# Kernel tuning notes

Measured on AMD Instinct MI355X. Metric: run time of the kernel, lower is better.

Reference implementation:

```python
import jax, jax.numpy as jnp
import numpy as np

N_NODES = 50000
N_EDGES = 800000
IN_FEATS, HIDDEN, OUT = 256, 64, 32


def graph_conv(x, W, b, src, dst, n_nodes):
    # DGL GraphConv with norm='both': h = D_in^{-1/2} A D_out^{-1/2} (x W) + b
    ones = jnp.ones((src.shape[0],), dtype=x.dtype)
    deg_out = jax.ops.segment_sum(ones, src, num_segments=n_nodes)
    deg_in = jax.ops.segment_sum(ones, dst, num_segments=n_nodes)
    norm_out = jax.lax.rsqrt(jnp.maximum(deg_out, 1.0))  # [N]
    norm_in = jax.lax.rsqrt(jnp.maximum(deg_in, 1.0))    # [N]
    xw = x @ W                                # [N, out] dense transform first
    msg = (xw * norm_out[:, None])[src]       # [E, out] gather
    agg = jax.ops.segment_sum(msg, dst, num_segments=n_nodes)  # [N, out]
    return agg * norm_in[:, None] + b


def setup_inputs() -> dict:
    key = jax.random.key(0)
    ks = jax.random.split(key, 9)
    inputs = jax.random.normal(ks[0], (N_NODES, IN_FEATS), dtype=jnp.float32)
    src = jax.random.randint(ks[1], (N_EDGES,), 0, N_NODES)
    dst = jax.random.randint(ks[2], (N_EDGES,), 0, N_NODES)
    W1 = jax.random.normal(ks[3], (IN_FEATS, HIDDEN), dtype=jnp.float32) / np.sqrt(IN_FEATS)
    b1 = jnp.zeros((HIDDEN,), dtype=jnp.float32)
    W2 = jax.random.normal(ks[4], (HIDDEN, OUT), dtype=jnp.float32) / np.sqrt(HIDDEN)
    b2 = jnp.zeros((OUT,), dtype=jnp.float32)
    fc_w = jax.random.normal(ks[5], (N_NODES,), dtype=jnp.float32) / np.sqrt(N_NODES)
    fc_b = jnp.zeros((1,), dtype=jnp.float32)
    return {"inputs": inputs, "src": src, "dst": dst,
            "W1": W1, "b1": b1, "W2": W2, "b2": b2,
            "fc_w": fc_w, "fc_b": fc_b}


def reference(inputs, src, dst, W1, b1, W2, b2, fc_w, fc_b):
    g1 = jax.nn.relu(graph_conv(inputs, W1, b1, src, dst, N_NODES))  # [N, H]
    g2 = jax.nn.relu(graph_conv(g1, W2, b2, src, dst, N_NODES))      # [N, O]
    # fc(g2.t()): Linear(nodes, 1) on [O, N] -> [O, 1]
    out = jnp.einsum('no,n->o', g2, fc_w)[:, None] + fc_b
    return out
```

## Files before the change

kernel.cpp:

```cpp
#include <hip/hip_runtime.h>

#define N_NODES 50000
#define N_EDGES 800000
#define IN_FEATS 256
#define HIDDEN 64
#define OUTF 32
#define SCAN_BLOCKS 196

#define NSLICE 64
#define SLICE_E 12500
#define NRANGE 4
#define RANGE_N 12800
#define PSTRIDE 51200

#define HRANGE 2
#define HRANGE_N 25600

typedef __attribute__((ext_vector_type(8))) short bf16x8;
typedef __attribute__((ext_vector_type(4))) float f32x4;
typedef unsigned short u16;

__device__ __forceinline__ unsigned f2bf_pk(float a, float b) {
    union { float f; unsigned u; } x, y;
    x.f = a; y.f = b;
    unsigned lo = x.u + 0x7FFFu + ((x.u >> 16) & 1u);
    unsigned hi = y.u + 0x7FFFu + ((y.u >> 16) & 1u);
    return (lo >> 16) | (hi & 0xFFFF0000u);
}
__device__ __forceinline__ u16 f2bf(float a) {
    union { float f; unsigned u; } x;
    x.f = a;
    return (u16)((x.u + 0x7FFFu + ((x.u >> 16) & 1u)) >> 16);
}
__device__ __forceinline__ float bf2f(u16 h) {
    union { unsigned u; float f; } x;
    x.u = ((unsigned)h) << 16;
    return x.f;
}

__global__ __launch_bounds__(512) void hist_kernel(const int* __restrict__ src,
                                                   const int* __restrict__ dst,
                                                   unsigned char* __restrict__ partial) {
    __shared__ int h[HRANGE_N / 2];
    const int bid = blockIdx.x;
    const int which = bid & 1;
    const int r = (bid >> 1) & 1;
    const int s = bid >> 2;
    const int tid = threadIdx.x;
    const int lo = r * HRANGE_N;

    for (int i = tid; i < HRANGE_N / 2; i += 512) h[i] = 0;
    __syncthreads();

    const int* arr = which ? dst : src;
    const int e0 = s * SLICE_E;
    for (int j = tid; j < SLICE_E; j += 512) {
        int v = arr[e0 + j] - lo;
        if ((unsigned)v < HRANGE_N) atomicAdd(&h[v >> 1], 1 << ((v & 1) << 4));
    }
    __syncthreads();

    unsigned char* p = partial + (size_t)which * NSLICE * PSTRIDE + (size_t)s * PSTRIDE + lo;
    for (int i = tid; i < HRANGE_N / 2; i += 512) {
        int c = h[i];
        p[i * 2 + 0] = (unsigned char)(c & 0xFFFF);
        p[i * 2 + 1] = (unsigned char)((unsigned)c >> 16);
    }
}

__global__ __launch_bounds__(256) void reduce_scan_kernel(unsigned char* __restrict__ partial,
                                                          int* __restrict__ row_start,
                                                          int* __restrict__ block_sums,
                                                          float* __restrict__ norm_out,
                                                          float* __restrict__ norm_in) {
    __shared__ int sh[256];
    int i = blockIdx.x * 256 + threadIdx.x;
    int run = 0;
    if (i < N_NODES) {
        const unsigned char* ps = partial + i;
        unsigned char* pd = partial + (size_t)NSLICE * PSTRIDE + i;
        int so = 0;
#pragma unroll 8
        for (int s = 0; s < NSLICE; ++s) so += ps[(size_t)s * PSTRIDE];
        norm_out[i] = rsqrtf(fmaxf((float)so, 1.0f));
#pragma unroll 8
        for (int s = 0; s < NSLICE; ++s) {
            int c = pd[(size_t)s * PSTRIDE];
            pd[(size_t)s * PSTRIDE] = (unsigned char)run;
            run += c;
        }
        norm_in[i] = rsqrtf(fmaxf((float)run, 1.0f));
    }
    sh[threadIdx.x] = run;
    __syncthreads();
#pragma unroll
    for (int off = 1; off < 256; off <<= 1) {
        int t = (threadIdx.x >= off) ? sh[threadIdx.x - off] : 0;
        __syncthreads();
        sh[threadIdx.x] += t;
        __syncthreads();
    }
    if (i < N_NODES) row_start[i] = sh[threadIdx.x] - run;
    if (threadIdx.x == 255) block_sums[blockIdx.x] = sh[255];
}

__global__ __launch_bounds__(256) void scan3_kernel(int* __restrict__ row_start,
                                                    const int* __restrict__ block_sums) {
    __shared__ int s[256];
    int v = (threadIdx.x < SCAN_BLOCKS) ? block_sums[threadIdx.x] : 0;
    s[threadIdx.x] = v;
    __syncthreads();
#pragma unroll
    for (int off = 1; off < 256; off <<= 1) {
        int t = (threadIdx.x >= off) ? s[threadIdx.x - off] : 0;
        __syncthreads();
        s[threadIdx.x] += t;
        __syncthreads();
    }
    int base = (blockIdx.x == 0) ? 0 : s[blockIdx.x - 1];
    int i = blockIdx.x * 256 + threadIdx.x;
    if (i < N_NODES) row_start[i] += base;
    if (i == 0) row_start[N_NODES] = N_EDGES;
}

__global__ __launch_bounds__(512) void fill_csr_kernel(const int* __restrict__ src,
                                                       const int* __restrict__ dst,
                                                       const int* __restrict__ row_start,
                                                       const unsigned char* __restrict__ rel,
                                                       int* __restrict__ csr_src) {
    __shared__ int cur[RANGE_N];
    const int bid = blockIdx.x;
    const int r = bid & 3;
    const int s = bid >> 2;
    const int tid = threadIdx.x;
    const int lo = r * RANGE_N;

    const unsigned char* relp = rel + (size_t)s * PSTRIDE;
    for (int i = tid; i < RANGE_N; i += 512) {
        int node = lo + i;
        cur[i] = (node < N_NODES) ? row_start[node] + (int)relp[node] : 0;
    }
    __syncthreads();

    const int e0 = s * SLICE_E;
    for (int j = tid; j < SLICE_E; j += 512) {
        int d = dst[e0 + j] - lo;
        if ((unsigned)d < RANGE_N) {
            int pos = atomicAdd(&cur[d], 1);
            csr_src[pos] = src[e0 + j];
        }
    }
}

#define AST 136
__global__ __launch_bounds__(256) void gemm1_kernel(const float* __restrict__ x,
                                                    const float* __restrict__ W1,
                                                    const float* __restrict__ norm_out,
                                                    u16* __restrict__ xw1) {
    __shared__ short As[64 * AST];
    __shared__ short Bt[64 * AST];
    const int tid = threadIdx.x;
    const int n0 = blockIdx.x * 64;

    const f32x4 zero4 = {0.f, 0.f, 0.f, 0.f};
    f32x4 acc[4] = {zero4, zero4, zero4, zero4};

    const int srow = tid >> 2;
    const int sseg = tid & 3;
    const int grow = n0 + srow;
    const bool grow_ok = grow < N_NODES;

    const int w = tid >> 6;
    const int l = tid & 63;

    for (int c = 0; c < 2; ++c) {
        if (c) __syncthreads();
        {
            const float* xp = x + (size_t)grow * IN_FEATS + c * 128 + sseg * 32;
            short* ap = As + srow * AST + sseg * 32;
#pragma unroll
            for (int j = 0; j < 8; ++j) {
                float4 v = make_float4(0.f, 0.f, 0.f, 0.f);
                if (grow_ok) v = *(const float4*)(xp + j * 4);
                unsigned p0 = f2bf_pk(v.x, v.y);
                unsigned p1 = f2bf_pk(v.z, v.w);
                *(uint2*)(ap + j * 4) = make_uint2(p0, p1);
            }
        }
        {
#pragma unroll
            for (int it = 0; it < 16; ++it) {
                int flat = tid + it * 256;
                int kp = flat >> 6;
                int col = flat & 63;
                int k = c * 128 + kp * 2;
                float w0 = W1[(size_t)k * HIDDEN + col];
                float w1 = W1[(size_t)(k + 1) * HIDDEN + col];
                *(unsigned*)(Bt + col * AST + kp * 2) = f2bf_pk(w0, w1);
            }
        }
        __syncthreads();

        const short* ap = As + (w * 16 + (l & 15)) * AST + (l >> 4) * 8;
        const short* bp = Bt + (l & 15) * AST + (l >> 4) * 8;
#pragma unroll
        for (int ks = 0; ks < 4; ++ks) {
            bf16x8 af = *(const bf16x8*)(ap + ks * 32);
#pragma unroll
            for (int ct = 0; ct < 4; ++ct) {
                bf16x8 bfv = *(const bf16x8*)(bp + ct * 16 * AST + ks * 32);
                acc[ct] = __builtin_amdgcn_mfma_f32_16x16x32_bf16(af, bfv, acc[ct], 0, 0, 0);
            }
        }
    }

    const int rbase = n0 + w * 16 + (l >> 4) * 4;
    const int cbase = l & 15;
#pragma unroll
    for (int j = 0; j < 4; ++j) {
        int row = rbase + j;
        if (row < N_NODES) {
            float nrm = norm_out[row];
            u16* orow = xw1 + (size_t)row * HIDDEN + cbase;
#pragma unroll
            for (int ct = 0; ct < 4; ++ct)
                orow[ct * 16] = f2bf(acc[ct][j] * nrm);
        }
    }
}

__global__ __launch_bounds__(256) void gemm2_kernel(const float* __restrict__ g1,
                                                    const float* __restrict__ W2,
                                                    const float* __restrict__ norm_out,
                                                    u16* __restrict__ xw2) {
    __shared__ float gs[8][HIDDEN];
    __shared__ float ws[HIDDEN * OUTF];
    const int tid = threadIdx.x;
    const int n0 = blockIdx.x * 8;

#pragma unroll
    for (int i = 0; i < 8; ++i) ws[tid + i * 256] = W2[tid + i * 256];
    const float4* gv = (const float4*)(g1 + (size_t)n0 * HIDDEN);
    if (tid < 128) ((float4*)&gs[0][0])[tid] = gv[tid];
    __syncthreads();

    const int o = tid & 31;
    const int r = tid >> 5;
    float acc = 0.f;
#pragma unroll
    for (int k = 0; k < HIDDEN; ++k) acc += gs[r][k] * ws[k * OUTF + o];
    xw2[(size_t)(n0 + r) * OUTF + o] = f2bf(acc * norm_out[n0 + r]);
}

__global__ __launch_bounds__(256) void gather64_kernel(const int* __restrict__ row_start,
                                                       const int* __restrict__ csr_src,
                                                       const u16* __restrict__ xw,
                                                       const float* __restrict__ norm_in,
                                                       const float* __restrict__ b,
                                                       float* __restrict__ g) {
    int n = blockIdx.x * 4 + (threadIdx.x >> 6);
    if (n >= N_NODES) return;
    int lane = threadIdx.x & 63;
    int beg = row_start[n], end = row_start[n + 1];
    float acc = 0.f;
    int i = beg;
    for (; i + 8 <= end; i += 8) {
        int s0 = csr_src[i + 0], s1 = csr_src[i + 1];
        int s2 = csr_src[i + 2], s3 = csr_src[i + 3];
        int s4 = csr_src[i + 4], s5 = csr_src[i + 5];
        int s6 = csr_src[i + 6], s7 = csr_src[i + 7];
        float v0 = bf2f(xw[(size_t)s0 * 64 + lane]);
        float v1 = bf2f(xw[(size_t)s1 * 64 + lane]);
        float v2 = bf2f(xw[(size_t)s2 * 64 + lane]);
        float v3 = bf2f(xw[(size_t)s3 * 64 + lane]);
        float v4 = bf2f(xw[(size_t)s4 * 64 + lane]);
        float v5 = bf2f(xw[(size_t)s5 * 64 + lane]);
        float v6 = bf2f(xw[(size_t)s6 * 64 + lane]);
        float v7 = bf2f(xw[(size_t)s7 * 64 + lane]);
        acc += ((v0 + v1) + (v2 + v3)) + ((v4 + v5) + (v6 + v7));
    }
    for (; i < end; ++i) acc += bf2f(xw[(size_t)csr_src[i] * 64 + lane]);
    g[(size_t)n * 64 + lane] = fmaxf(acc * norm_in[n] + b[lane], 0.f);
}

__global__ __launch_bounds__(256) void gather32_kernel(const int* __restrict__ row_start,
                                                       const int* __restrict__ csr_src,
                                                       const u16* __restrict__ xw,
                                                       const float* __restrict__ norm_in,
                                                       const float* __restrict__ b,
                                                       float* __restrict__ g) {
    int n = blockIdx.x * 8 + (threadIdx.x >> 5);
    if (n >= N_NODES) return;
    int lane = threadIdx.x & 31;
    int beg = row_start[n], end = row_start[n + 1];
    float acc = 0.f;
    int i = beg;
    for (; i + 8 <= end; i += 8) {
        int s0 = csr_src[i + 0], s1 = csr_src[i + 1];
        int s2 = csr_src[i + 2], s3 = csr_src[i + 3];
        int s4 = csr_src[i + 4], s5 = csr_src[i + 5];
        int s6 = csr_src[i + 6], s7 = csr_src[i + 7];
        float v0 = bf2f(xw[(size_t)s0 * 32 + lane]);
        float v1 = bf2f(xw[(size_t)s1 * 32 + lane]);
        float v2 = bf2f(xw[(size_t)s2 * 32 + lane]);
        float v3 = bf2f(xw[(size_t)s3 * 32 + lane]);
        float v4 = bf2f(xw[(size_t)s4 * 32 + lane]);
        float v5 = bf2f(xw[(size_t)s5 * 32 + lane]);
        float v6 = bf2f(xw[(size_t)s6 * 32 + lane]);
        float v7 = bf2f(xw[(size_t)s7 * 32 + lane]);
        acc += ((v0 + v1) + (v2 + v3)) + ((v4 + v5) + (v6 + v7));
    }
    for (; i < end; ++i) acc += bf2f(xw[(size_t)csr_src[i] * 32 + lane]);
    g[(size_t)n * 32 + lane] = fmaxf(acc * norm_in[n] + b[lane], 0.f);
}

__global__ __launch_bounds__(32) void init_out_kernel(float* __restrict__ out,
                                                      const float* __restrict__ fc_b) {
    out[threadIdx.x] = fc_b[0];
}

__global__ __launch_bounds__(256) void reduce_kernel(const float* __restrict__ g2,
                                                     const float* __restrict__ fc_w,
                                                     float* __restrict__ out) {
    __shared__ float s[OUTF];
    const int tid = threadIdx.x;
    if (tid < OUTF) s[tid] = 0.f;
    __syncthreads();

    const int f4 = tid & 7;
    int n = blockIdx.x * 32 + (tid >> 3);
    const int stride = gridDim.x * 32;
    float ax = 0.f, ay = 0.f, az = 0.f, aw = 0.f;
    for (; n < N_NODES; n += stride) {
        float w = fc_w[n];
        float4 g = ((const float4*)(g2 + (size_t)n * OUTF))[f4];
        ax += g.x * w; ay += g.y * w; az += g.z * w; aw += g.w * w;
    }
    atomicAdd(&s[f4 * 4 + 0], ax);
    atomicAdd(&s[f4 * 4 + 1], ay);
    atomicAdd(&s[f4 * 4 + 2], az);
    atomicAdd(&s[f4 * 4 + 3], aw);
    __syncthreads();
    if (tid < OUTF) atomicAdd(&out[tid], s[tid]);
}

extern "C" void kernel_launch(void* const* d_in, const int* in_sizes, int n_in,
                              void* d_out, int out_size, void* d_ws, size_t ws_size,
                              hipStream_t stream) {
    const float* x    = (const float*)d_in[0];
    const int*   src  = (const int*)d_in[1];
    const int*   dst  = (const int*)d_in[2];
    const float* W1   = (const float*)d_in[3];
    const float* b1   = (const float*)d_in[4];
    const float* W2   = (const float*)d_in[5];
    const float* b2   = (const float*)d_in[6];
    const float* fc_w = (const float*)d_in[7];
    const float* fc_b = (const float*)d_in[8];
    float* out = (float*)d_out;

    int* ip = (int*)d_ws;
    int* csr_src      = ip;
    int* row_start    = ip + 800000;
    int* block_sums   = ip + 850001;
    float* fp = (float*)(ip + 850260);
    u16* xw_buf     = (u16*)fp;
    float* g_buf    = fp + 3200000;
    float* norm_out = fp + 6400000;
    float* norm_in  = fp + 6450000;
    unsigned char* partial = (unsigned char*)(fp + 6500000);
    unsigned char* rel = partial + (size_t)NSLICE * PSTRIDE;

    hist_kernel<<<NSLICE * HRANGE * 2, 512, 0, stream>>>(src, dst, partial);
    reduce_scan_kernel<<<SCAN_BLOCKS, 256, 0, stream>>>(partial, row_start, block_sums,
                                                        norm_out, norm_in);
    scan3_kernel<<<SCAN_BLOCKS, 256, 0, stream>>>(row_start, block_sums);
    fill_csr_kernel<<<NSLICE * NRANGE, 512, 0, stream>>>(src, dst, row_start, rel, csr_src);

    gemm1_kernel<<<(N_NODES + 63) / 64, 256, 0, stream>>>(x, W1, norm_out, xw_buf);
    gather64_kernel<<<(N_NODES + 3) / 4, 256, 0, stream>>>(row_start, csr_src, xw_buf,
                                                           norm_in, b1, g_buf);

    gemm2_kernel<<<N_NODES / 8, 256, 0, stream>>>(g_buf, W2, norm_out, xw_buf);
    gather32_kernel<<<(N_NODES + 7) / 8, 256, 0, stream>>>(row_start, csr_src, xw_buf,
                                                           norm_in, b2, g_buf);

    init_out_kernel<<<1, 32, 0, stream>>>(out, fc_b);
    reduce_kernel<<<512, 256, 0, stream>>>(g_buf, fc_w, out);
}
```

Measured before the change: 160.8 us.

## Fuse gathers with gemm2 and final reduction, use 16-bit CSR indices

The layer-1 gather is fused with the layer-2 dense transform, so the hidden features stay in shared memory instead of passing through a global fp32 buffer. The layer-2 gather is fused with the fc reduction, so g2 is never written to global memory. CSR source indices are stored as u16, which is valid only because the node count is below 65536. Gathers now load two bf16 values per lane and split edges across half-waves, with shuffle reductions to combine them. Together these remove two kernel launches and several global round trips, at the cost of more complex indexing and extra shuffles.

```diff
diff --git a/kernel.cpp b/kernel.cpp
--- a/kernel.cpp
+++ b/kernel.cpp
@@ -32,10 +32,11 @@
     x.f = a;
     return (u16)((x.u + 0x7FFFu + ((x.u >> 16) & 1u)) >> 16);
 }
-__device__ __forceinline__ float bf2f(u16 h) {
-    union { unsigned u; float f; } x;
-    x.u = ((unsigned)h) << 16;
-    return x.f;
+__device__ __forceinline__ float bflo(unsigned v) {
+    union { unsigned u; float f; } x; x.u = v << 16; return x.f;
+}
+__device__ __forceinline__ float bfhi(unsigned v) {
+    union { unsigned u; float f; } x; x.u = v & 0xFFFF0000u; return x.f;
 }
 
 __global__ __launch_bounds__(512) void hist_kernel(const int* __restrict__ src,
@@ -127,7 +128,7 @@
                                                        const int* __restrict__ dst,
                                                        const int* __restrict__ row_start,
                                                        const unsigned char* __restrict__ rel,
-                                                       int* __restrict__ csr_src) {
+                                                       u16* __restrict__ csr16) {
     __shared__ int cur[RANGE_N];
     const int bid = blockIdx.x;
     const int r = bid & 3;
@@ -147,7 +148,7 @@
         int d = dst[e0 + j] - lo;
         if ((unsigned)d < RANGE_N) {
             int pos = atomicAdd(&cur[d], 1);
-            csr_src[pos] = src[e0 + j];
+            csr16[pos] = (u16)src[e0 + j];
         }
     }
 }
@@ -229,119 +230,143 @@
     }
 }
 
-__global__ __launch_bounds__(256) void gemm2_kernel(const float* __restrict__ g1,
-                                                    const float* __restrict__ W2,
-                                                    const float* __restrict__ norm_out,
-                                                    u16* __restrict__ xw2) {
-    __shared__ float gs[8][HIDDEN];
+__global__ __launch_bounds__(256) void gather64_gemm2_kernel(const int* __restrict__ row_start,
+                                                             const u16* __restrict__ csr16,
+                                                             const u16* __restrict__ xw1,
+                                                             const float* __restrict__ norm_in,
+                                                             const float* __restrict__ b1,
+                                                             const float* __restrict__ W2,
+                                                             const float* __restrict__ norm_out,
+                                                             u16* __restrict__ xw2) {
+    __shared__ float gs[16][68];
     __shared__ float ws[HIDDEN * OUTF];
     const int tid = threadIdx.x;
-    const int n0 = blockIdx.x * 8;
-
 #pragma unroll
     for (int i = 0; i < 8; ++i) ws[tid + i * 256] = W2[tid + i * 256];
-    const float4* gv = (const float4*)(g1 + (size_t)n0 * HIDDEN);
-    if (tid < 128) ((float4*)&gs[0][0])[tid] = gv[tid];
+
+    const int w = tid >> 6;
+    const int l = tid & 63;
+    const int p = l & 31;
+    const int gsl = l >> 5;
+    const int n0 = blockIdx.x * 16;
+
+#pragma unroll
+    for (int i4 = 0; i4 < 4; ++i4) {
+        int nl = w * 4 + i4;
+        int n = n0 + nl;
+        int beg = row_start[n], end = row_start[n + 1];
+        float ax = 0.f, ay = 0.f;
+        int i = beg;
+        for (; i + 8 <= end; i += 8) {
+            int s0 = csr16[i + gsl];
+            int s1 = csr16[i + 2 + gsl];
+            int s2 = csr16[i + 4 + gsl];
+            int s3 = csr16[i + 6 + gsl];
+            unsigned v0 = *(const unsigned*)(xw1 + (size_t)s0 * 64 + 2 * p);
+            unsigned v1 = *(const unsigned*)(xw1 + (size_t)s1 * 64 + 2 * p);
+            unsigned v2 = *(const unsigned*)(xw1 + (size_t)s2 * 64 + 2 * p);
+            unsigned v3 = *(const unsigned*)(xw1 + (size_t)s3 * 64 + 2 * p);
+            ax += (bflo(v0) + bflo(v1)) + (bflo(v2) + bflo(v3));
+            ay += (bfhi(v0) + bfhi(v1)) + (bfhi(v2) + bfhi(v3));
+        }
+        for (; i + 2 <= end; i += 2) {
+            int s0 = csr16[i + gsl];
+            unsigned v0 = *(const unsigned*)(xw1 + (size_t)s0 * 64 + 2 * p);
+            ax += bflo(v0);
+            ay += bfhi(v0);
+        }
+        if (i < end && gsl == 0) {
+            int s0 = csr16[i];
+            unsigned v0 = *(const unsigned*)(xw1 + (size_t)s0 * 64 + 2 * p);
+            ax += bflo(v0);
+            ay += bfhi(v0);
+        }
+        ax += __shfl_xor(ax, 32);
+        ay += __shfl_xor(ay, 32);
+        if (gsl == 0) {
+            float nin = norm_in[n];
+            gs[nl][2 * p]     = fmaxf(ax * nin + b1[2 * p], 0.f);
+            gs[nl][2 * p + 1] = fmaxf(ay * nin + b1[2 * p + 1], 0.f);
+        }
+    }
     __syncthreads();
 
     const int o = tid & 31;
     const int r = tid >> 5;
-    float acc = 0.f;
-#pragma unroll
-    for (int k = 0; k < HIDDEN; ++k) acc += gs[r][k] * ws[k * OUTF + o];
-    xw2[(size_t)(n0 + r) * OUTF + o] = f2bf(acc * norm_out[n0 + r]);
-}
-
-__global__ __launch_bounds__(256) void gather64_kernel(const int* __restrict__ row_start,
-                                                       const int* __restrict__ csr_src,
-                                                       const u16* __restrict__ xw,
-                                                       const float* __restrict__ norm_in,
-                                                       const float* __restrict__ b,
-                                                       float* __restrict__ g) {
-    int n = blockIdx.x * 4 + (threadIdx.x >> 6);
-    if (n >= N_NODES) return;
-    int lane = threadIdx.x & 63;
-    int beg = row_start[n], end = row_start[n + 1];
-    float acc = 0.f;
-    int i = beg;
-    for (; i + 8 <= end; i += 8) {
-        int s0 = csr_src[i + 0], s1 = csr_src[i + 1];
-        int s2 = csr_src[i + 2], s3 = csr_src[i + 3];
-        int s4 = csr_src[i + 4], s5 = csr_src[i + 5];
-        int s6 = csr_src[i + 6], s7 = csr_src[i + 7];
-        float v0 = bf2f(xw[(size_t)s0 * 64 + lane]);
-        float v1 = bf2f(xw[(size_t)s1 * 64 + lane]);
-        float v2 = bf2f(xw[(size_t)s2 * 64 + lane]);
-        float v3 = bf2f(xw[(size_t)s3 * 64 + lane]);
-        float v4 = bf2f(xw[(size_t)s4 * 64 + lane]);
-        float v5 = bf2f(xw[(size_t)s5 * 64 + lane]);
-        float v6 = bf2f(xw[(size_t)s6 * 64 + lane]);
-        float v7 = bf2f(xw[(size_t)s7 * 64 + lane]);
-        acc += ((v0 + v1) + (v2 + v3)) + ((v4 + v5) + (v6 + v7));
-    }
-    for (; i < end; ++i) acc += bf2f(xw[(size_t)csr_src[i] * 64 + lane]);
-    g[(size_t)n * 64 + lane] = fmaxf(acc * norm_in[n] + b[lane], 0.f);
-}
-
-__global__ __launch_bounds__(256) void gather32_kernel(const int* __restrict__ row_start,
-                                                       const int* __restrict__ csr_src,
-                                                       const u16* __restrict__ xw,
-                                                       const float* __restrict__ norm_in,
-                                                       const float* __restrict__ b,
-                                                       float* __restrict__ g) {
-    int n = blockIdx.x * 8 + (threadIdx.x >> 5);
-    if (n >= N_NODES) return;
-    int lane = threadIdx.x & 31;
-    int beg = row_start[n], end = row_start[n + 1];
-    float acc = 0.f;
-    int i = beg;
-    for (; i + 8 <= end; i += 8) {
-        int s0 = csr_src[i + 0], s1 = csr_src[i + 1];
-        int s2 = csr_src[i + 2], s3 = csr_src[i + 3];
-        int s4 = csr_src[i + 4], s5 = csr_src[i + 5];
-        int s6 = csr_src[i + 6], s7 = csr_src[i + 7];
-        float v0 = bf2f(xw[(size_t)s0 * 32 + lane]);
-        float v1 = bf2f(xw[(size_t)s1 * 32 + lane]);
-        float v2 = bf2f(xw[(size_t)s2 * 32 + lane]);
-        float v3 = bf2f(xw[(size_t)s3 * 32 + lane]);
-        float v4 = bf2f(xw[(size_t)s4 * 32 + lane]);
-        float v5 = bf2f(xw[(size_t)s5 * 32 + lane]);
-        float v6 = bf2f(xw[(size_t)s6 * 32 + lane]);
-        float v7 = bf2f(xw[(size_t)s7 * 32 + lane]);
-        acc += ((v0 + v1) + (v2 + v3)) + ((v4 + v5) + (v6 + v7));
-    }
-    for (; i < end; ++i) acc += bf2f(xw[(size_t)csr_src[i] * 32 + lane]);
-    g[(size_t)n * 32 + lane] = fmaxf(acc * norm_in[n] + b[lane], 0.f);
+    float a0 = 0.f, a1 = 0.f;
+#pragma unroll 8
+    for (int k = 0; k < 64; ++k) {
+        float wv = ws[k * 32 + o];
+        a0 += gs[r][k] * wv;
+        a1 += gs[r + 8][k] * wv;
+    }
+    int row0 = n0 + r, row1 = n0 + r + 8;
+    xw2[(size_t)row0 * 32 + o] = f2bf(a0 * norm_out[row0]);
+    xw2[(size_t)row1 * 32 + o] = f2bf(a1 * norm_out[row1]);
+}
+
+__global__ __launch_bounds__(256) void gather32_reduce_kernel(const int* __restrict__ row_start,
+                                                              const u16* __restrict__ csr16,
+                                                              const u16* __restrict__ xw2,
+                                                              const float* __restrict__ norm_in,
+                                                              const float* __restrict__ b2,
+                                                              const float* __restrict__ fc_w,
+                                                              float* __restrict__ out) {
+    __shared__ float sout[OUTF];
+    const int tid = threadIdx.x;
+    if (tid < OUTF) sout[tid] = 0.f;
+    __syncthreads();
+
+    const int w = tid >> 6;
+    const int l = tid & 63;
+    const int p = l & 15;
+    const int gsl = l >> 4;
+    float tx = 0.f, ty = 0.f;
+
+    for (int n = blockIdx.x * 4 + w; n < N_NODES; n += gridDim.x * 4) {
+        int beg = row_start[n], end = row_start[n + 1];
+        float ax = 0.f, ay = 0.f;
+        int i = beg;
+        for (; i + 8 <= end; i += 8) {
+            int s0 = csr16[i + gsl];
+            int s1 = csr16[i + 4 + gsl];
+            unsigned v0 = *(const unsigned*)(xw2 + (size_t)s0 * 32 + 2 * p);
+            unsigned v1 = *(const unsigned*)(xw2 + (size_t)s1 * 32 + 2 * p);
+            ax += bflo(v0) + bflo(v1);
+            ay += bfhi(v0) + bfhi(v1);
+        }
+        for (; i + 4 <= end; i += 4) {
+            int s0 = csr16[i + gsl];
+            unsigned v0 = *(const unsigned*)(xw2 + (size_t)s0 * 32 + 2 * p);
+            ax += bflo(v0);
+            ay += bfhi(v0);
+        }
+        int t = end - i;
+        if (gsl < t) {
+            int s0 = csr16[i + gsl];
+            unsigned v0 = *(const unsigned*)(xw2 + (size_t)s0 * 32 + 2 * p);
+            ax += bflo(v0);
+            ay += bfhi(v0);
+        }
+        ax += __shfl_xor(ax, 16); ax += __shfl_xor(ax, 32);
+        ay += __shfl_xor(ay, 16); ay += __shfl_xor(ay, 32);
+        if (gsl == 0) {
+            float nin = norm_in[n], fw = fc_w[n];
+            tx += fmaxf(ax * nin + b2[2 * p], 0.f) * fw;
+            ty += fmaxf(ay * nin + b2[2 * p + 1], 0.f) * fw;
+        }
+    }
+    if (gsl == 0) {
+        atomicAdd(&sout[2 * p], tx);
+        atomicAdd(&sout[2 * p + 1], ty);
+    }
+    __syncthreads();
+    if (tid < OUTF) atomicAdd(&out[tid], sout[tid]);
 }
 
 __global__ __launch_bounds__(32) void init_out_kernel(float* __restrict__ out,
                                                       const float* __restrict__ fc_b) {
     out[threadIdx.x] = fc_b[0];
-}
-
-__global__ __launch_bounds__(256) void reduce_kernel(const float* __restrict__ g2,
-                                                     const float* __restrict__ fc_w,
-                                                     float* __restrict__ out) {
-    __shared__ float s[OUTF];
-    const int tid = threadIdx.x;
-    if (tid < OUTF) s[tid] = 0.f;
-    __syncthreads();
-
-    const int f4 = tid & 7;
-    int n = blockIdx.x * 32 + (tid >> 3);
-    const int stride = gridDim.x * 32;
-    float ax = 0.f, ay = 0.f, az = 0.f, aw = 0.f;
-    for (; n < N_NODES; n += stride) {
-        float w = fc_w[n];
-        float4 g = ((const float4*)(g2 + (size_t)n * OUTF))[f4];
-        ax += g.x * w; ay += g.y * w; az += g.z * w; aw += g.w * w;
-    }
-    atomicAdd(&s[f4 * 4 + 0], ax);
-    atomicAdd(&s[f4 * 4 + 1], ay);
-    atomicAdd(&s[f4 * 4 + 2], az);
-    atomicAdd(&s[f4 * 4 + 3], aw);
-    __syncthreads();
-    if (tid < OUTF) atomicAdd(&out[tid], s[tid]);
 }
 
 extern "C" void kernel_launch(void* const* d_in, const int* in_sizes, int n_in,
@@ -358,32 +383,29 @@
     const float* fc_b = (const float*)d_in[8];
     float* out = (float*)d_out;
 
-    int* ip = (int*)d_ws;
-    int* csr_src      = ip;
-    int* row_start    = ip + 800000;
-    int* block_sums   = ip + 850001;
-    float* fp = (float*)(ip + 850260);
-    u16* xw_buf     = (u16*)fp;
-    float* g_buf    = fp + 3200000;
-    float* norm_out = fp + 6400000;
-    float* norm_in  = fp + 6450000;
-    unsigned char* partial = (unsigned char*)(fp + 6500000);
+    u16* csr16      = (u16*)d_ws;
+    int* row_start  = (int*)(csr16 + 800000);
+    int* block_sums = row_start + 50004;
+    u16* xw1_buf    = (u16*)(block_sums + 260);
+    u16* xw2_buf    = xw1_buf + 3200000;
+    float* norm_out = (float*)(xw2_buf + 1600000);
+    float* norm_in  = norm_out + 50000;
+    unsigned char* partial = (unsigned char*)(norm_in + 50000);
     unsigned char* rel = partial + (size_t)NSLICE * PSTRIDE;
 
     hist_kernel<<<NSLICE * HRANGE * 2, 512, 0, stream>>>(src, dst, partial);
     reduce_scan_kernel<<<SCAN_BLOCKS, 256, 0, stream>>>(partial, row_start, block_sums,
                                                         norm_out, norm_in);
     scan3_kernel<<<SCAN_BLOCKS, 256, 0, stream>>>(row_start, block_sums);
-    fill_csr_kernel<<<NSLICE * NRANGE, 512, 0, stream>>>(src, dst, row_start, rel, csr_src);
-
-    gemm1_kernel<<<(N_NODES + 63) / 64, 256, 0, stream>>>(x, W1, norm_out, xw_buf);
-    gather64_kernel<<<(N_NODES + 3) / 4, 256, 0, stream>>>(row_start, csr_src, xw_buf,
-                                                           norm_in, b1, g_buf);
-
-    gemm2_kernel<<<N_NODES / 8, 256, 0, stream>>>(g_buf, W2, norm_out, xw_buf);
-    gather32_kernel<<<(N_NODES + 7) / 8, 256, 0, stream>>>(row_start, csr_src, xw_buf,
-                                                           norm_in, b2, g_buf);
+    fill_csr_kernel<<<NSLICE * NRANGE, 512, 0, stream>>>(src, dst, row_start, rel, csr16);
+
+    gemm1_kernel<<<(N_NODES + 63) / 64, 256, 0, stream>>>(x, W1, norm_out, xw1_buf);
+
+    gather64_gemm2_kernel<<<N_NODES / 16, 256, 0, stream>>>(row_start, csr16, xw1_buf,
+                                                            norm_in, b1, W2, norm_out,
+                                                            xw2_buf);
 
     init_out_kernel<<<1, 32, 0, stream>>>(out, fc_b);
-    reduce_kernel<<<512, 256, 0, stream>>>(g_buf, fc_w, out);
-}
+    gather32_reduce_kernel<<<512, 256, 0, stream>>>(row_start, csr16, xw2_buf,
+                                                    norm_in, b2, fc_w, out);
+}
```

Result: slower. 164.6 us (+2.4%).
